# Optimization experiments

Measured on AMD Instinct MI355X. Metric: run time of the kernel, lower is better.

## Reference

```python
import jax, jax.numpy as jnp
import numpy as np

S, B, H, T = 512, 64, 512, 32

def setup_inputs() -> dict:
    key = jax.random.key(0)
    ks = jax.random.split(key, 6)
    hidden = jax.random.normal(ks[0], (S, B, H), jnp.float32)
    lens = jax.random.randint(ks[1], (B,), 1, S + 1)  # sentence lengths in [1, S]
    masks = jnp.ones((S, B), jnp.bool_)  # unused (attention is None), kept for signature parity
    W1 = jax.random.normal(ks[2], (H, H), jnp.float32) / np.sqrt(H)
    b1 = jnp.zeros((H,), jnp.float32)
    W2 = jax.random.normal(ks[3], (H, T), jnp.float32) / np.sqrt(H)
    b2 = jnp.zeros((T,), jnp.float32)
    # xavier_normal_ init for transition
    transition = jax.random.normal(ks[4], (T, T), jnp.float32) * np.sqrt(2.0 / (T + T))
    return {"hidden": hidden, "lens": lens, "masks": masks,
            "W1": W1, "b1": b1, "W2": W2, "b2": b2, "transition": transition}


def _viterbi(emissions, lens, transition):
    # emissions: [S, B, T]; transition[curr, prev]
    Sdim, Bdim, Tn = emissions.shape
    ident = jnp.broadcast_to(jnp.arange(Tn), (Bdim, Tn))  # identity backpointers for padded steps

    def step(fv, inp):
        em_t, t = inp
        scores = fv[:, None, :] + transition[None, :, :]  # [B, curr, prev]
        bp = jnp.argmax(scores, axis=-1)                  # [B, T]
        new_fv = jnp.max(scores, axis=-1) + em_t          # [B, T]
        active = (t < lens)[:, None]
        fv = jnp.where(active, new_fv, fv)                # freeze state past sentence end
        bp = jnp.where(active, bp, ident)
        return fv, bp

    fv0 = emissions[0]
    ts = jnp.arange(1, Sdim)
    fv, bps = jax.lax.scan(step, fv0, (emissions[1:], ts))  # bps: [S-1, B, T]
    best_id = jnp.argmax(fv, axis=-1)   # [B]
    best_score = jnp.max(fv, axis=-1)   # [B]

    def back(tag, bp_t):
        prev = jnp.take_along_axis(bp_t, tag[:, None], axis=1)[:, 0]
        return prev, prev

    _, prevs = jax.lax.scan(back, best_id, bps, reverse=True)  # [S-1, B]
    paths = jnp.concatenate([prevs, best_id[None]], axis=0)    # [S, B]; beyond len-1 the tag repeats
    return paths, best_score


def reference(hidden, lens, masks, W1, b1, W2, b2, transition):
    # hidden2emission: Linear -> Sigmoid -> Linear
    h1 = jax.nn.sigmoid(hidden @ W1 + b1)   # [S, B, H]
    emissions = h1 @ W2 + b2                # [S, B, T]
    paths, best_score = _viterbi(emissions, lens, transition)
    return paths, best_score
```

## Files before the change

### kernel.cpp

```cpp
#include <hip/hip_runtime.h>
#include <math.h>

#define SDIM 512
#define BDIM 64
#define HDIM 512
#define TDIM 32
#define MTOT (SDIM * BDIM)

typedef __attribute__((ext_vector_type(8))) short bf16x8;
typedef __attribute__((ext_vector_type(4))) float f32x4;

__device__ unsigned short g_w1hT[HDIM * HDIM];
__device__ unsigned short g_w1lT[HDIM * HDIM];
__device__ unsigned short g_w2hT[TDIM * HDIM];
__device__ unsigned short g_w2lT[TDIM * HDIM];
__device__ float g_em[(size_t)MTOT * TDIM];

__device__ __forceinline__ unsigned short f2bf(float x) {
  union { float f; unsigned int u; } v; v.f = x;
  unsigned int r = v.u + 0x7FFFu + ((v.u >> 16) & 1u);
  return (unsigned short)(r >> 16);
}
__device__ __forceinline__ float bf2f(unsigned short h) {
  union { float f; unsigned int u; } v; v.u = ((unsigned int)h) << 16; return v.f;
}
__device__ __forceinline__ float fmax3(float a, float b, float c) {
  return fmaxf(fmaxf(a, b), c);
}
__device__ __forceinline__ int imin3(int a, int b, int c) {
  int m = a < b ? a : b; return m < c ? m : c;
}

__global__ void split_kernel(const float* __restrict__ W1, const float* __restrict__ W2) {
  const int n = blockIdx.x;
  const int k0 = threadIdx.x * 4;
  if (n < HDIM) {
    ushort4 h, l; float x;
    x = W1[(size_t)(k0 + 0) * HDIM + n]; h.x = f2bf(x); l.x = f2bf(x - bf2f(h.x));
    x = W1[(size_t)(k0 + 1) * HDIM + n]; h.y = f2bf(x); l.y = f2bf(x - bf2f(h.y));
    x = W1[(size_t)(k0 + 2) * HDIM + n]; h.z = f2bf(x); l.z = f2bf(x - bf2f(h.z));
    x = W1[(size_t)(k0 + 3) * HDIM + n]; h.w = f2bf(x); l.w = f2bf(x - bf2f(h.w));
    *(ushort4*)&g_w1hT[(size_t)n * HDIM + k0] = h;
    *(ushort4*)&g_w1lT[(size_t)n * HDIM + k0] = l;
  } else {
    const int t = n - HDIM;
    ushort4 h, l; float x;
    x = W2[(size_t)(k0 + 0) * TDIM + t]; h.x = f2bf(x); l.x = f2bf(x - bf2f(h.x));
    x = W2[(size_t)(k0 + 1) * TDIM + t]; h.y = f2bf(x); l.y = f2bf(x - bf2f(h.y));
    x = W2[(size_t)(k0 + 2) * TDIM + t]; h.z = f2bf(x); l.z = f2bf(x - bf2f(h.z));
    x = W2[(size_t)(k0 + 3) * TDIM + t]; h.w = f2bf(x); l.w = f2bf(x - bf2f(h.w));
    *(ushort4*)&g_w2hT[(size_t)t * HDIM + k0] = h;
    *(ushort4*)&g_w2lT[(size_t)t * HDIM + k0] = l;
  }
}

__global__ __launch_bounds__(256) void emis_kernel(
    const float* __restrict__ hidden, const float* __restrict__ b1,
    const float* __restrict__ b2)
{
  __shared__ unsigned short lAh[64][40];
  __shared__ unsigned short lAl[64][40];
  __shared__ unsigned short lBh[128][40];
  __shared__ unsigned short lBl[128][40];
  __shared__ unsigned short H1h[64][136];
  __shared__ unsigned short H1l[64][136];

  const int tid = threadIdx.x;
  const int s = blockIdx.x;
  const int row0 = s * 64;
  const int wave = tid >> 6;
  const int lane = tid & 63;
  const int l15 = lane & 15;
  const int l4 = lane >> 4;
  const int wr1 = (wave >> 1) * 32;
  const int wc1 = (wave & 1) * 64;

  f32x4 acc_em[2];
  acc_em[0] = (f32x4)(0.f);
  acc_em[1] = (f32x4)(0.f);

  for (int jcb = 0; jcb < 4; ++jcb) {
    const int jc = jcb * 128;

    f32x4 acc1[2][4];
#pragma unroll
    for (int i = 0; i < 2; ++i)
#pragma unroll
      for (int j = 0; j < 4; ++j) acc1[i][j] = (f32x4)(0.f);

    for (int k0 = 0; k0 < HDIM; k0 += 32) {
#pragma unroll
      for (int i = 0; i < 2; ++i) {
        int f4 = tid + 256 * i;
        int r = f4 >> 3, q = f4 & 7;
        float4 v = *(const float4*)&hidden[(size_t)(row0 + r) * HDIM + k0 + 4 * q];
        ushort4 h, l;
        h.x = f2bf(v.x); l.x = f2bf(v.x - bf2f(h.x));
        h.y = f2bf(v.y); l.y = f2bf(v.y - bf2f(h.y));
        h.z = f2bf(v.z); l.z = f2bf(v.z - bf2f(h.z));
        h.w = f2bf(v.w); l.w = f2bf(v.w - bf2f(h.w));
        *(ushort4*)&lAh[r][4 * q] = h;
        *(ushort4*)&lAl[r][4 * q] = l;
      }
#pragma unroll
      for (int i = 0; i < 2; ++i) {
        int f8 = tid + 256 * i;
        int nl = f8 >> 2, kq8 = f8 & 3;
        *(uint4*)&lBh[nl][8 * kq8] =
            *(const uint4*)&g_w1hT[(size_t)(jc + nl) * HDIM + k0 + 8 * kq8];
        *(uint4*)&lBl[nl][8 * kq8] =
            *(const uint4*)&g_w1lT[(size_t)(jc + nl) * HDIM + k0 + 8 * kq8];
      }
      __syncthreads();

      bf16x8 aH[2], aL[2];
#pragma unroll
      for (int i = 0; i < 2; ++i) {
        aH[i] = *(const bf16x8*)&lAh[wr1 + 16 * i + l15][8 * l4];
        aL[i] = *(const bf16x8*)&lAl[wr1 + 16 * i + l15][8 * l4];
      }
#pragma unroll
      for (int j = 0; j < 4; ++j) {
        bf16x8 bH = *(const bf16x8*)&lBh[wc1 + 16 * j + l15][8 * l4];
        bf16x8 bL = *(const bf16x8*)&lBl[wc1 + 16 * j + l15][8 * l4];
#pragma unroll
        for (int i = 0; i < 2; ++i) {
          acc1[i][j] = __builtin_amdgcn_mfma_f32_16x16x32_bf16(aH[i], bH, acc1[i][j], 0, 0, 0);
          acc1[i][j] = __builtin_amdgcn_mfma_f32_16x16x32_bf16(aH[i], bL, acc1[i][j], 0, 0, 0);
          acc1[i][j] = __builtin_amdgcn_mfma_f32_16x16x32_bf16(aL[i], bH, acc1[i][j], 0, 0, 0);
        }
      }
      __syncthreads();
    }

#pragma unroll
    for (int j = 0; j < 4; ++j) {
      const int col = wc1 + 16 * j + l15;
      const float bv = b1[jc + col];
#pragma unroll
      for (int i = 0; i < 2; ++i) {
#pragma unroll
        for (int r = 0; r < 4; ++r) {
          int lrow = wr1 + 16 * i + 4 * l4 + r;
          float h = 1.f / (1.f + expf(-(acc1[i][j][r] + bv)));
          unsigned short hh = f2bf(h);
          unsigned short hl = f2bf(h - bf2f(hh));
          H1h[lrow][col] = hh;
          H1l[lrow][col] = hl;
        }
      }
    }
    __syncthreads();

#pragma unroll
    for (int ks = 0; ks < 4; ++ks) {
      bf16x8 aH2 = *(const bf16x8*)&H1h[16 * wave + l15][32 * ks + 8 * l4];
      bf16x8 aL2 = *(const bf16x8*)&H1l[16 * wave + l15][32 * ks + 8 * l4];
#pragma unroll
      for (int j2 = 0; j2 < 2; ++j2) {
        const size_t wo = (size_t)(16 * j2 + l15) * HDIM + jc + 32 * ks + 8 * l4;
        bf16x8 bH2 = *(const bf16x8*)&g_w2hT[wo];
        bf16x8 bL2 = *(const bf16x8*)&g_w2lT[wo];
        acc_em[j2] = __builtin_amdgcn_mfma_f32_16x16x32_bf16(aH2, bH2, acc_em[j2], 0, 0, 0);
        acc_em[j2] = __builtin_amdgcn_mfma_f32_16x16x32_bf16(aH2, bL2, acc_em[j2], 0, 0, 0);
        acc_em[j2] = __builtin_amdgcn_mfma_f32_16x16x32_bf16(aL2, bH2, acc_em[j2], 0, 0, 0);
      }
    }
    __syncthreads();
  }

#pragma unroll
  for (int j2 = 0; j2 < 2; ++j2) {
    const int t = 16 * j2 + l15;
    const float bv = b2[t];
#pragma unroll
    for (int r = 0; r < 4; ++r) {
      int b = 16 * wave + 4 * l4 + r;
      g_em[((size_t)b * SDIM + s) * TDIM + t] = acc_em[j2][r] + bv;
    }
  }
}

__global__ __launch_bounds__(64) void viterbi_kernel(
    const int* __restrict__ lens, const float* __restrict__ trans,
    float* __restrict__ out)
{
  __shared__ float fvL[64];
  __shared__ unsigned int bps32[SDIM / 4][TDIM];
  const int b = blockIdx.x;
  const int lane = threadIdx.x;
  const int c = lane & 31;
  const int h = lane >> 5;
  const int p0 = 16 * h;

  float tr[16];
#pragma unroll
  for (int j = 0; j < 16; j += 4) {
    float4 t4 = *(const float4*)&trans[c * TDIM + p0 + j];
    tr[j] = t4.x; tr[j + 1] = t4.y; tr[j + 2] = t4.z; tr[j + 3] = t4.w;
  }

  int len;
  { const int* p32 = lens;
    len = (p32[1] == 0) ? (int)((const long long*)lens)[b] : p32[b]; }

  const float* emc = g_em + (size_t)b * SDIM * TDIM + c;

  float fvown = emc[0];
  fvL[lane] = fvown;

  float ebuf[12];
#pragma unroll
  for (int j = 0; j < 12; ++j) ebuf[j] = emc[(size_t)(1 + j) * TDIM];

  unsigned int bpk = 0u;

#define VSTEP(T, PH, EV)                                                       \
  {                                                                            \
    float4 q0 = *(const float4*)&fvL[p0];                                      \
    float4 q1 = *(const float4*)&fvL[p0 + 4];                                  \
    float4 q2 = *(const float4*)&fvL[p0 + 8];                                  \
    float4 q3 = *(const float4*)&fvL[p0 + 12];                                 \
    float sv[16];                                                              \
    sv[0] = q0.x + tr[0];  sv[1] = q0.y + tr[1];                               \
    sv[2] = q0.z + tr[2];  sv[3] = q0.w + tr[3];                               \
    sv[4] = q1.x + tr[4];  sv[5] = q1.y + tr[5];                               \
    sv[6] = q1.z + tr[6];  sv[7] = q1.w + tr[7];                               \
    sv[8] = q2.x + tr[8];  sv[9] = q2.y + tr[9];                               \
    sv[10] = q2.z + tr[10]; sv[11] = q2.w + tr[11];                            \
    sv[12] = q3.x + tr[12]; sv[13] = q3.y + tr[13];                            \
    sv[14] = q3.z + tr[14]; sv[15] = q3.w + tr[15];                            \
    float l0 = fmax3(sv[0], sv[1], sv[2]);                                     \
    float l1 = fmax3(sv[3], sv[4], sv[5]);                                     \
    float l2 = fmax3(sv[6], sv[7], sv[8]);                                     \
    float l3 = fmax3(sv[9], sv[10], sv[11]);                                   \
    float l4 = fmax3(sv[12], sv[13], sv[14]);                                  \
    float mh = fmaxf(fmax3(l0, l1, l2), fmax3(l3, l4, sv[15]));                \
    float mo = __shfl_xor(mh, 32, 64);                                         \
    float m0 = fmaxf(mh, mo);                                                  \
    const bool act = (T) < len;                                                \
    fvown = act ? (m0 + (EV)) : fvown;                                         \
    fvL[lane] = fvown;       \
    int i_[16];                                                                \
    _Pragma("unroll")                                                          \
    for (int j = 0; j < 16; ++j) i_[j] = (sv[j] == m0) ? j : 63;               \
    int u0 = imin3(i_[0], i_[1], i_[2]);                                       \
    int u1 = imin3(i_[3], i_[4], i_[5]);                                       \
    int u2 = imin3(i_[6], i_[7], i_[8]);                                       \
    int u3 = imin3(i_[9], i_[10], i_[11]);                                     \
    int u4 = imin3(i_[12], i_[13], i_[14]);                                    \
    int jm = imin3(imin3(u0, u1, u2), imin3(u3, u4, i_[15]), 63);              \
    int gi = (jm == 63) ? 255 : (p0 + jm);                                     \
    int go = __shfl_xor(gi, 32, 64);                                           \
    int im = gi < go ? gi : go;                                                \
    int bp = act ? im : c;                                                     \
    bpk |= (unsigned)bp << (8 * (PH));                                         \
    if ((PH) == 3) { bps32[(T) >> 2][c] = bpk; bpk = 0u; }                     \
  }

#define LOADQ(BASE, T0)                                                        \
  {                                                                            \
    _Pragma("unroll")                                                          \
    for (int j = 0; j < 4; ++j) {                                              \
      int lt = (T0) + j; lt = lt > (SDIM - 1) ? (SDIM - 1) : lt;               \
      ebuf[(BASE) + j] = emc[(size_t)lt * TDIM];                               \
    }                                                                          \
  }

  {
    int tq = 1;
    for (; tq <= SDIM - 19; tq += 12) {
      VSTEP(tq + 0, 1, ebuf[0]) VSTEP(tq + 1, 2, ebuf[1])
      VSTEP(tq + 2, 3, ebuf[2]) VSTEP(tq + 3, 0, ebuf[3])
      LOADQ(0, tq + 12)
      VSTEP(tq + 4, 1, ebuf[4]) VSTEP(tq + 5, 2, ebuf[5])
      VSTEP(tq + 6, 3, ebuf[6]) VSTEP(tq + 7, 0, ebuf[7])
      LOADQ(4, tq + 16)
      VSTEP(tq + 8, 1, ebuf[8]) VSTEP(tq + 9, 2, ebuf[9])
      VSTEP(tq + 10, 3, ebuf[10]) VSTEP(tq + 11, 0, ebuf[11])
      LOADQ(8, tq + 20)
    }
    VSTEP(505, 1, ebuf[0]) VSTEP(506, 2, ebuf[1]) VSTEP(507, 3, ebuf[2])
    VSTEP(508, 0, ebuf[3]) VSTEP(509, 1, ebuf[4]) VSTEP(510, 2, ebuf[5])
    VSTEP(511, 3, ebuf[6])
  }
#undef VSTEP
#undef LOADQ

  float bs = fvown;
  int bi = c;
#pragma unroll
  for (int off = 16; off > 0; off >>= 1) {
    float os = __shfl_down(bs, off, 32);
    int oi = __shfl_down(bi, off, 32);
    if (os > bs || (os == bs && oi < bi)) { bs = os; bi = oi; }
  }
  bs = __shfl(bs, 0, 32);
  int tag = __shfl(bi, 0, 32);

  out[(size_t)SDIM * BDIM + b] = bs;
  out[(size_t)(SDIM - 1) * BDIM + b] = (float)tag;

  unsigned bw_next = bps32[SDIM / 4 - 1][c];
  for (int w = SDIM / 4 - 1; w >= 0; --w) {
    unsigned bw = bw_next;
    if (w > 0) bw_next = bps32[w - 1][c];
#pragma unroll
    for (int j = 3; j >= 0; --j) {
      int t = 4 * w + j;
      if (t < 1) continue;
      unsigned word = (unsigned)__builtin_amdgcn_readlane((int)bw, tag);
      tag = (int)((word >> (8 * j)) & 255u);
      out[(size_t)(t - 1) * BDIM + b] = (float)tag;
    }
  }
}

static int find_by_size(const int* in_sizes, int n_in, int sz, int fb) {
  for (int i = 0; i < n_in; ++i) if (in_sizes[i] == sz) return i;
  return fb;
}

extern "C" void kernel_launch(void* const* d_in, const int* in_sizes, int n_in,
                              void* d_out, int out_size, void* d_ws, size_t ws_size,
                              hipStream_t stream) {
  const int i_hidden = find_by_size(in_sizes, n_in, SDIM * BDIM * HDIM, 0);
  const int i_lens   = find_by_size(in_sizes, n_in, BDIM, 1);
  const int i_W1     = find_by_size(in_sizes, n_in, HDIM * HDIM, 3);
  const int i_b1     = find_by_size(in_sizes, n_in, HDIM, 4);
  const int i_W2     = find_by_size(in_sizes, n_in, HDIM * TDIM, 5);
  const int i_b2     = find_by_size(in_sizes, n_in, TDIM, 6);
  const int i_tr     = find_by_size(in_sizes, n_in, TDIM * TDIM, 7);

  const float* hidden = (const float*)d_in[i_hidden];
  const int*   lens   = (const int*)d_in[i_lens];
  const float* W1     = (const float*)d_in[i_W1];
  const float* b1     = (const float*)d_in[i_b1];
  const float* W2     = (const float*)d_in[i_W2];
  const float* b2     = (const float*)d_in[i_b2];
  const float* trans  = (const float*)d_in[i_tr];
  float* out = (float*)d_out;

  split_kernel<<<HDIM + TDIM, 128, 0, stream>>>(W1, W2);
  emis_kernel<<<SDIM, 256, 0, stream>>>(hidden, b1, b2);
  viterbi_kernel<<<BDIM, 64, 0, stream>>>(lens, trans, out);
}
```

Baseline: 239.4 us.

## Pre-split hidden into bf16 hi/lo buffers; widen Viterbi lanes to full row

Adds a split_hidden kernel that converts the whole hidden tensor into bf16 hi/lo arrays once, so the GEMM kernel no longer reconverts the same A tile for each of its four column blocks. The cost is an extra full pass that writes and rereads 64 MB. The sigmoid now uses the fast __expf intrinsic. The Viterbi step has each lane handle all 32 previous tags instead of splitting them across two half-waves, which removes the cross-lane shuffles but doubles per-lane work and leaves half the lanes computing redundantly.

```diff
diff --git a/kernel.cpp b/kernel.cpp
--- a/kernel.cpp
+++ b/kernel.cpp
@@ -14,6 +14,8 @@
 __device__ unsigned short g_w1lT[HDIM * HDIM];
 __device__ unsigned short g_w2hT[TDIM * HDIM];
 __device__ unsigned short g_w2lT[TDIM * HDIM];
+__device__ unsigned short g_aH[(size_t)MTOT * HDIM];
+__device__ unsigned short g_aL[(size_t)MTOT * HDIM];
 __device__ float g_em[(size_t)MTOT * TDIM];
 
 __device__ __forceinline__ unsigned short f2bf(float x) {
@@ -54,9 +56,24 @@
   }
 }
 
+__global__ __launch_bounds__(256) void split_hidden(const float* __restrict__ hidden) {
+  const size_t base = (size_t)blockIdx.x * 4096 + threadIdx.x * 4;
+#pragma unroll
+  for (int i = 0; i < 4; ++i) {
+    size_t idx = base + (size_t)i * 1024;
+    float4 v = *(const float4*)&hidden[idx];
+    ushort4 h, l;
+    h.x = f2bf(v.x); l.x = f2bf(v.x - bf2f(h.x));
+    h.y = f2bf(v.y); l.y = f2bf(v.y - bf2f(h.y));
+    h.z = f2bf(v.z); l.z = f2bf(v.z - bf2f(h.z));
+    h.w = f2bf(v.w); l.w = f2bf(v.w - bf2f(h.w));
+    *(ushort4*)&g_aH[idx] = h;
+    *(ushort4*)&g_aL[idx] = l;
+  }
+}
+
 __global__ __launch_bounds__(256) void emis_kernel(
-    const float* __restrict__ hidden, const float* __restrict__ b1,
-    const float* __restrict__ b2)
+    const float* __restrict__ b1, const float* __restrict__ b2)
 {
   __shared__ unsigned short lAh[64][40];
   __shared__ unsigned short lAl[64][40];
@@ -79,6 +96,8 @@
   acc_em[0] = (f32x4)(0.f);
   acc_em[1] = (f32x4)(0.f);
 
+  const int ar = tid >> 2, aq = tid & 3;
+
   for (int jcb = 0; jcb < 4; ++jcb) {
     const int jc = jcb * 128;
 
@@ -89,18 +108,10 @@
       for (int j = 0; j < 4; ++j) acc1[i][j] = (f32x4)(0.f);
 
     for (int k0 = 0; k0 < HDIM; k0 += 32) {
-#pragma unroll
-      for (int i = 0; i < 2; ++i) {
-        int f4 = tid + 256 * i;
-        int r = f4 >> 3, q = f4 & 7;
-        float4 v = *(const float4*)&hidden[(size_t)(row0 + r) * HDIM + k0 + 4 * q];
-        ushort4 h, l;
-        h.x = f2bf(v.x); l.x = f2bf(v.x - bf2f(h.x));
-        h.y = f2bf(v.y); l.y = f2bf(v.y - bf2f(h.y));
-        h.z = f2bf(v.z); l.z = f2bf(v.z - bf2f(h.z));
-        h.w = f2bf(v.w); l.w = f2bf(v.w - bf2f(h.w));
-        *(ushort4*)&lAh[r][4 * q] = h;
-        *(ushort4*)&lAl[r][4 * q] = l;
+      {
+        const size_t ao = (size_t)(row0 + ar) * HDIM + k0 + 8 * aq;
+        *(uint4*)&lAh[ar][8 * aq] = *(const uint4*)&g_aH[ao];
+        *(uint4*)&lAl[ar][8 * aq] = *(const uint4*)&g_aL[ao];
       }
 #pragma unroll
       for (int i = 0; i < 2; ++i) {
@@ -142,7 +153,7 @@
 #pragma unroll
         for (int r = 0; r < 4; ++r) {
           int lrow = wr1 + 16 * i + 4 * l4 + r;
-          float h = 1.f / (1.f + expf(-(acc1[i][j][r] + bv)));
+          float h = 1.f / (1.f + __expf(-(acc1[i][j][r] + bv)));
           unsigned short hh = f2bf(h);
           unsigned short hl = f2bf(h - bf2f(hh));
           H1h[lrow][col] = hh;
@@ -190,14 +201,12 @@
   const int b = blockIdx.x;
   const int lane = threadIdx.x;
   const int c = lane & 31;
-  const int h = lane >> 5;
-  const int p0 = 16 * h;
-
-  float tr[16];
-#pragma unroll
-  for (int j = 0; j < 16; j += 4) {
-    float4 t4 = *(const float4*)&trans[c * TDIM + p0 + j];
-    tr[j] = t4.x; tr[j + 1] = t4.y; tr[j + 2] = t4.z; tr[j + 3] = t4.w;
+
+  float tr[TDIM];
+#pragma unroll
+  for (int p = 0; p < TDIM; p += 4) {
+    float4 t4 = *(const float4*)&trans[c * TDIM + p];
+    tr[p] = t4.x; tr[p + 1] = t4.y; tr[p + 2] = t4.z; tr[p + 3] = t4.w;
   }
 
   int len;
@@ -217,11 +226,15 @@
 
 #define VSTEP(T, PH, EV)                                                       \
   {                                                                            \
-    float4 q0 = *(const float4*)&fvL[p0];                                      \
-    float4 q1 = *(const float4*)&fvL[p0 + 4];                                  \
-    float4 q2 = *(const float4*)&fvL[p0 + 8];                                  \
-    float4 q3 = *(const float4*)&fvL[p0 + 12];                                 \
-    float sv[16];                                                              \
+    float4 q0 = *(const float4*)&fvL[0];                                       \
+    float4 q1 = *(const float4*)&fvL[4];                                       \
+    float4 q2 = *(const float4*)&fvL[8];                                       \
+    float4 q3 = *(const float4*)&fvL[12];                                      \
+    float4 q4 = *(const float4*)&fvL[16];                                      \
+    float4 q5 = *(const float4*)&fvL[20];                                      \
+    float4 q6 = *(const float4*)&fvL[24];                                      \
+    float4 q7 = *(const float4*)&fvL[28];                                      \
+    float sv[32];                                                              \
     sv[0] = q0.x + tr[0];  sv[1] = q0.y + tr[1];                               \
     sv[2] = q0.z + tr[2];  sv[3] = q0.w + tr[3];                               \
     sv[4] = q1.x + tr[4];  sv[5] = q1.y + tr[5];                               \
@@ -230,29 +243,52 @@
     sv[10] = q2.z + tr[10]; sv[11] = q2.w + tr[11];                            \
     sv[12] = q3.x + tr[12]; sv[13] = q3.y + tr[13];                            \
     sv[14] = q3.z + tr[14]; sv[15] = q3.w + tr[15];                            \
-    float l0 = fmax3(sv[0], sv[1], sv[2]);                                     \
-    float l1 = fmax3(sv[3], sv[4], sv[5]);                                     \
-    float l2 = fmax3(sv[6], sv[7], sv[8]);                                     \
-    float l3 = fmax3(sv[9], sv[10], sv[11]);                                   \
-    float l4 = fmax3(sv[12], sv[13], sv[14]);                                  \
-    float mh = fmaxf(fmax3(l0, l1, l2), fmax3(l3, l4, sv[15]));                \
-    float mo = __shfl_xor(mh, 32, 64);                                         \
-    float m0 = fmaxf(mh, mo);                                                  \
+    sv[16] = q4.x + tr[16]; sv[17] = q4.y + tr[17];                            \
+    sv[18] = q4.z + tr[18]; sv[19] = q4.w + tr[19];                            \
+    sv[20] = q5.x + tr[20]; sv[21] = q5.y + tr[21];                            \
+    sv[22] = q5.z + tr[22]; sv[23] = q5.w + tr[23];                            \
+    sv[24] = q6.x + tr[24]; sv[25] = q6.y + tr[25];                            \
+    sv[26] = q6.z + tr[26]; sv[27] = q6.w + tr[27];                            \
+    sv[28] = q7.x + tr[28]; sv[29] = q7.y + tr[29];                            \
+    sv[30] = q7.z + tr[30]; sv[31] = q7.w + tr[31];                            \
+    float a0 = fmax3(sv[0], sv[1], sv[2]);                                     \
+    float a1 = fmax3(sv[3], sv[4], sv[5]);                                     \
+    float a2 = fmax3(sv[6], sv[7], sv[8]);                                     \
+    float a3 = fmax3(sv[9], sv[10], sv[11]);                                   \
+    float a4 = fmax3(sv[12], sv[13], sv[14]);                                  \
+    float a5 = fmax3(sv[15], sv[16], sv[17]);                                  \
+    float a6 = fmax3(sv[18], sv[19], sv[20]);                                  \
+    float a7 = fmax3(sv[21], sv[22], sv[23]);                                  \
+    float a8 = fmax3(sv[24], sv[25], sv[26]);                                  \
+    float a9 = fmax3(sv[27], sv[28], sv[29]);                                  \
+    float a10 = fmaxf(sv[30], sv[31]);                                         \
+    float b0 = fmax3(a0, a1, a2);                                              \
+    float b1_ = fmax3(a3, a4, a5);                                             \
+    float b2_ = fmax3(a6, a7, a8);                                             \
+    float b3_ = fmaxf(a9, a10);                                                \
+    float m0 = fmaxf(fmaxf(b0, b1_), fmaxf(b2_, b3_));                         \
     const bool act = (T) < len;                                                \
     fvown = act ? (m0 + (EV)) : fvown;                                         \
-    fvL[lane] = fvown;       \
-    int i_[16];                                                                \
+    fvL[lane] = fvown;   \
+    int i_[32];                                                                \
     _Pragma("unroll")                                                          \
-    for (int j = 0; j < 16; ++j) i_[j] = (sv[j] == m0) ? j : 63;               \
+    for (int j = 0; j < 32; ++j) i_[j] = (sv[j] == m0) ? j : 63;               \
     int u0 = imin3(i_[0], i_[1], i_[2]);                                       \
     int u1 = imin3(i_[3], i_[4], i_[5]);                                       \
     int u2 = imin3(i_[6], i_[7], i_[8]);                                       \
     int u3 = imin3(i_[9], i_[10], i_[11]);                                     \
     int u4 = imin3(i_[12], i_[13], i_[14]);                                    \
-    int jm = imin3(imin3(u0, u1, u2), imin3(u3, u4, i_[15]), 63);              \
-    int gi = (jm == 63) ? 255 : (p0 + jm);                                     \
-    int go = __shfl_xor(gi, 32, 64);                                           \
-    int im = gi < go ? gi : go;                                                \
+    int u5 = imin3(i_[15], i_[16], i_[17]);                                    \
+    int u6 = imin3(i_[18], i_[19], i_[20]);                                    \
+    int u7 = imin3(i_[21], i_[22], i_[23]);                                    \
+    int u8 = imin3(i_[24], i_[25], i_[26]);                                    \
+    int u9 = imin3(i_[27], i_[28], i_[29]);                                    \
+    int ua = i_[30] < i_[31] ? i_[30] : i_[31];                                \
+    int w0 = imin3(u0, u1, u2);                                                \
+    int w1 = imin3(u3, u4, u5);                                                \
+    int w2 = imin3(u6, u7, u8);                                                \
+    int w3 = u9 < ua ? u9 : ua;                                                \
+    int im = imin3(w0, w1, w2) < w3 ? imin3(w0, w1, w2) : w3;                  \
     int bp = act ? im : c;                                                     \
     bpk |= (unsigned)bp << (8 * (PH));                                         \
     if ((PH) == 3) { bps32[(T) >> 2][c] = bpk; bpk = 0u; }                     \
@@ -342,6 +378,7 @@
   float* out = (float*)d_out;
 
   split_kernel<<<HDIM + TDIM, 128, 0, stream>>>(W1, W2);
-  emis_kernel<<<SDIM, 256, 0, stream>>>(hidden, b1, b2);
+  split_hidden<<<(MTOT * HDIM) / 4096, 256, 0, stream>>>(hidden);
+  emis_kernel<<<SDIM, 256, 0, stream>>>(b1, b2);
   viterbi_kernel<<<BDIM, 64, 0, stream>>>(lens, trans, out);
 }
```

New measurement: 305.0 us. 27.4% more time.

## Interleave two batch rows per Viterbi wavefront and use fast exp in sigmoid

Applied to the files above, without the earlier changes.

The Viterbi kernel now processes two sentences per 64-lane block, interleaving their independent max/argmax recurrences so each step's LDS, shuffle and ALU latency can overlap across the two chains. Launch count halves to 32 blocks, and backtrace stores are limited to lane 0. The sigmoid in the emission GEMM switches expf to __expf for cheaper transcendental evaluation. The interleaving lengthens each block's dependent chain work and reduces block-level parallelism. The fast exp slightly changes emission precision, which could alter argmax ties.

```diff
diff --git a/kernel.cpp b/kernel.cpp
--- a/kernel.cpp
+++ b/kernel.cpp
@@ -142,7 +142,7 @@
 #pragma unroll
         for (int r = 0; r < 4; ++r) {
           int lrow = wr1 + 16 * i + 4 * l4 + r;
-          float h = 1.f / (1.f + expf(-(acc1[i][j][r] + bv)));
+          float h = 1.f / (1.f + __expf(-(acc1[i][j][r] + bv)));
           unsigned short hh = f2bf(h);
           unsigned short hl = f2bf(h - bf2f(hh));
           H1h[lrow][col] = hh;
@@ -185,13 +185,15 @@
     const int* __restrict__ lens, const float* __restrict__ trans,
     float* __restrict__ out)
 {
-  __shared__ float fvL[64];
-  __shared__ unsigned int bps32[SDIM / 4][TDIM];
-  const int b = blockIdx.x;
+  __shared__ float fvLA[64];
+  __shared__ float fvLB[64];
+  __shared__ unsigned int bps32[2][SDIM / 4][TDIM];
   const int lane = threadIdx.x;
   const int c = lane & 31;
   const int h = lane >> 5;
   const int p0 = 16 * h;
+  const int bA = 2 * blockIdx.x;
+  const int bB = bA + 1;
 
   float tr[16];
 #pragma unroll
@@ -200,62 +202,111 @@
     tr[j] = t4.x; tr[j + 1] = t4.y; tr[j + 2] = t4.z; tr[j + 3] = t4.w;
   }
 
-  int len;
+  int lenA, lenB;
   { const int* p32 = lens;
-    len = (p32[1] == 0) ? (int)((const long long*)lens)[b] : p32[b]; }
-
-  const float* emc = g_em + (size_t)b * SDIM * TDIM + c;
-
-  float fvown = emc[0];
-  fvL[lane] = fvown;
-
-  float ebuf[12];
-#pragma unroll
-  for (int j = 0; j < 12; ++j) ebuf[j] = emc[(size_t)(1 + j) * TDIM];
-
-  unsigned int bpk = 0u;
-
-#define VSTEP(T, PH, EV)                                                       \
+    if (p32[1] == 0) {
+      lenA = (int)((const long long*)lens)[bA];
+      lenB = (int)((const long long*)lens)[bB];
+    } else { lenA = p32[bA]; lenB = p32[bB]; } }
+
+  const float* emcA = g_em + (size_t)bA * SDIM * TDIM + c;
+  const float* emcB = g_em + (size_t)bB * SDIM * TDIM + c;
+
+  float fvA = emcA[0];
+  float fvB = emcB[0];
+  fvLA[lane] = fvA;
+  fvLB[lane] = fvB;
+
+  float ebA[12], ebB[12];
+#pragma unroll
+  for (int j = 0; j < 12; ++j) {
+    ebA[j] = emcA[(size_t)(1 + j) * TDIM];
+    ebB[j] = emcB[(size_t)(1 + j) * TDIM];
+  }
+
+  unsigned int bpkA = 0u, bpkB = 0u;
+
+#define VSTEP(T, PH, EVA, EVB)                                                 \
   {                                                                            \
-    float4 q0 = *(const float4*)&fvL[p0];                                      \
-    float4 q1 = *(const float4*)&fvL[p0 + 4];                                  \
-    float4 q2 = *(const float4*)&fvL[p0 + 8];                                  \
-    float4 q3 = *(const float4*)&fvL[p0 + 12];                                 \
-    float sv[16];                                                              \
-    sv[0] = q0.x + tr[0];  sv[1] = q0.y + tr[1];                               \
-    sv[2] = q0.z + tr[2];  sv[3] = q0.w + tr[3];                               \
-    sv[4] = q1.x + tr[4];  sv[5] = q1.y + tr[5];                               \
-    sv[6] = q1.z + tr[6];  sv[7] = q1.w + tr[7];                               \
-    sv[8] = q2.x + tr[8];  sv[9] = q2.y + tr[9];                               \
-    sv[10] = q2.z + tr[10]; sv[11] = q2.w + tr[11];                            \
-    sv[12] = q3.x + tr[12]; sv[13] = q3.y + tr[13];                            \
-    sv[14] = q3.z + tr[14]; sv[15] = q3.w + tr[15];                            \
-    float l0 = fmax3(sv[0], sv[1], sv[2]);                                     \
-    float l1 = fmax3(sv[3], sv[4], sv[5]);                                     \
-    float l2 = fmax3(sv[6], sv[7], sv[8]);                                     \
-    float l3 = fmax3(sv[9], sv[10], sv[11]);                                   \
-    float l4 = fmax3(sv[12], sv[13], sv[14]);                                  \
-    float mh = fmaxf(fmax3(l0, l1, l2), fmax3(l3, l4, sv[15]));                \
-    float mo = __shfl_xor(mh, 32, 64);                                         \
-    float m0 = fmaxf(mh, mo);                                                  \
-    const bool act = (T) < len;                                                \
-    fvown = act ? (m0 + (EV)) : fvown;                                         \
-    fvL[lane] = fvown;       \
-    int i_[16];                                                                \
+    float4 aq0 = *(const float4*)&fvLA[p0];                                    \
+    float4 aq1 = *(const float4*)&fvLA[p0 + 4];                                \
+    float4 aq2 = *(const float4*)&fvLA[p0 + 8];                                \
+    float4 aq3 = *(const float4*)&fvLA[p0 + 12];                               \
+    float4 bq0 = *(const float4*)&fvLB[p0];                                    \
+    float4 bq1 = *(const float4*)&fvLB[p0 + 4];                                \
+    float4 bq2 = *(const float4*)&fvLB[p0 + 8];                                \
+    float4 bq3 = *(const float4*)&fvLB[p0 + 12];                               \
+    float svA[16], svB[16];                                                    \
+    svA[0] = aq0.x + tr[0];  svA[1] = aq0.y + tr[1];                           \
+    svA[2] = aq0.z + tr[2];  svA[3] = aq0.w + tr[3];                           \
+    svA[4] = aq1.x + tr[4];  svA[5] = aq1.y + tr[5];                           \
+    svA[6] = aq1.z + tr[6];  svA[7] = aq1.w + tr[7];                           \
+    svA[8] = aq2.x + tr[8];  svA[9] = aq2.y + tr[9];                           \
+    svA[10] = aq2.z + tr[10]; svA[11] = aq2.w + tr[11];                        \
+    svA[12] = aq3.x + tr[12]; svA[13] = aq3.y + tr[13];                        \
+    svA[14] = aq3.z + tr[14]; svA[15] = aq3.w + tr[15];                        \
+    svB[0] = bq0.x + tr[0];  svB[1] = bq0.y + tr[1];                           \
+    svB[2] = bq0.z + tr[2];  svB[3] = bq0.w + tr[3];                           \
+    svB[4] = bq1.x + tr[4];  svB[5] = bq1.y + tr[5];                           \
+    svB[6] = bq1.z + tr[6];  svB[7] = bq1.w + tr[7];                           \
+    svB[8] = bq2.x + tr[8];  svB[9] = bq2.y + tr[9];                           \
+    svB[10] = bq2.z + tr[10]; svB[11] = bq2.w + tr[11];                        \
+    svB[12] = bq3.x + tr[12]; svB[13] = bq3.y + tr[13];                        \
+    svB[14] = bq3.z + tr[14]; svB[15] = bq3.w + tr[15];                        \
+    float lA0 = fmax3(svA[0], svA[1], svA[2]);                                 \
+    float lA1 = fmax3(svA[3], svA[4], svA[5]);                                 \
+    float lA2 = fmax3(svA[6], svA[7], svA[8]);                                 \
+    float lA3 = fmax3(svA[9], svA[10], svA[11]);                               \
+    float lA4 = fmax3(svA[12], svA[13], svA[14]);                              \
+    float mhA = fmaxf(fmax3(lA0, lA1, lA2), fmax3(lA3, lA4, svA[15]));         \
+    float lB0 = fmax3(svB[0], svB[1], svB[2]);                                 \
+    float lB1 = fmax3(svB[3], svB[4], svB[5]);                                 \
+    float lB2 = fmax3(svB[6], svB[7], svB[8]);                                 \
+    float lB3 = fmax3(svB[9], svB[10], svB[11]);                               \
+    float lB4 = fmax3(svB[12], svB[13], svB[14]);                              \
+    float mhB = fmaxf(fmax3(lB0, lB1, lB2), fmax3(lB3, lB4, svB[15]));         \
+    float moA = __shfl_xor(mhA, 32, 64);                                       \
+    float moB = __shfl_xor(mhB, 32, 64);                                       \
+    float m0A = fmaxf(mhA, moA);                                               \
+    float m0B = fmaxf(mhB, moB);                                               \
+    const bool actA = (T) < lenA;                                              \
+    const bool actB = (T) < lenB;                                              \
+    fvA = actA ? (m0A + (EVA)) : fvA;                                          \
+    fvB = actB ? (m0B + (EVB)) : fvB;                                          \
+    fvLA[lane] = fvA;                                                          \
+    fvLB[lane] = fvB;                                                          \
+    int iA_[16], iB_[16];                                                      \
     _Pragma("unroll")                                                          \
-    for (int j = 0; j < 16; ++j) i_[j] = (sv[j] == m0) ? j : 63;               \
-    int u0 = imin3(i_[0], i_[1], i_[2]);                                       \
-    int u1 = imin3(i_[3], i_[4], i_[5]);                                       \
-    int u2 = imin3(i_[6], i_[7], i_[8]);                                       \
-    int u3 = imin3(i_[9], i_[10], i_[11]);                                     \
-    int u4 = imin3(i_[12], i_[13], i_[14]);                                    \
-    int jm = imin3(imin3(u0, u1, u2), imin3(u3, u4, i_[15]), 63);              \
-    int gi = (jm == 63) ? 255 : (p0 + jm);                                     \
-    int go = __shfl_xor(gi, 32, 64);                                           \
-    int im = gi < go ? gi : go;                                                \
-    int bp = act ? im : c;                                                     \
-    bpk |= (unsigned)bp << (8 * (PH));                                         \
-    if ((PH) == 3) { bps32[(T) >> 2][c] = bpk; bpk = 0u; }                     \
+    for (int j = 0; j < 16; ++j) iA_[j] = (svA[j] == m0A) ? j : 63;            \
+    _Pragma("unroll")                                                          \
+    for (int j = 0; j < 16; ++j) iB_[j] = (svB[j] == m0B) ? j : 63;            \
+    int uA0 = imin3(iA_[0], iA_[1], iA_[2]);                                   \
+    int uA1 = imin3(iA_[3], iA_[4], iA_[5]);                                   \
+    int uA2 = imin3(iA_[6], iA_[7], iA_[8]);                                   \
+    int uA3 = imin3(iA_[9], iA_[10], iA_[11]);                                 \
+    int uA4 = imin3(iA_[12], iA_[13], iA_[14]);                                \
+    int jmA = imin3(imin3(uA0, uA1, uA2), imin3(uA3, uA4, iA_[15]), 63);       \
+    int uB0 = imin3(iB_[0], iB_[1], iB_[2]);                                   \
+    int uB1 = imin3(iB_[3], iB_[4], iB_[5]);                                   \
+    int uB2 = imin3(iB_[6], iB_[7], iB_[8]);                                   \
+    int uB3 = imin3(iB_[9], iB_[10], iB_[11]);                                 \
+    int uB4 = imin3(iB_[12], iB_[13], iB_[14]);                                \
+    int jmB = imin3(imin3(uB0, uB1, uB2), imin3(uB3, uB4, iB_[15]), 63);       \
+    int giA = (jmA == 63) ? 255 : (p0 + jmA);                                  \
+    int giB = (jmB == 63) ? 255 : (p0 + jmB);                                  \
+    int goA = __shfl_xor(giA, 32, 64);                                         \
+    int goB = __shfl_xor(giB, 32, 64);                                         \
+    int imA = giA < goA ? giA : goA;                                           \
+    int imB = giB < goB ? giB : goB;                                           \
+    int bpA = actA ? imA : c;                                                  \
+    int bpB = actB ? imB : c;                                                  \
+    bpkA |= (unsigned)bpA << (8 * (PH));                                       \
+    bpkB |= (unsigned)bpB << (8 * (PH));                                       \
+    if ((PH) == 3) {                                                           \
+      bps32[0][(T) >> 2][c] = bpkA;                                            \
+      bps32[1][(T) >> 2][c] = bpkB;                                            \
+      bpkA = 0u; bpkB = 0u;                                                    \
+    }                                                                          \
   }
 
 #define LOADQ(BASE, T0)                                                        \
@@ -263,55 +314,71 @@
     _Pragma("unroll")                                                          \
     for (int j = 0; j < 4; ++j) {                                              \
       int lt = (T0) + j; lt = lt > (SDIM - 1) ? (SDIM - 1) : lt;               \
-      ebuf[(BASE) + j] = emc[(size_t)lt * TDIM];                               \
+      ebA[(BASE) + j] = emcA[(size_t)lt * TDIM];                               \
+      ebB[(BASE) + j] = emcB[(size_t)lt * TDIM];                               \
     }                                                                          \
   }
 
   {
     int tq = 1;
     for (; tq <= SDIM - 19; tq += 12) {
-      VSTEP(tq + 0, 1, ebuf[0]) VSTEP(tq + 1, 2, ebuf[1])
-      VSTEP(tq + 2, 3, ebuf[2]) VSTEP(tq + 3, 0, ebuf[3])
+      VSTEP(tq + 0, 1, ebA[0], ebB[0]) VSTEP(tq + 1, 2, ebA[1], ebB[1])
+      VSTEP(tq + 2, 3, ebA[2], ebB[2]) VSTEP(tq + 3, 0, ebA[3], ebB[3])
       LOADQ(0, tq + 12)
-      VSTEP(tq + 4, 1, ebuf[4]) VSTEP(tq + 5, 2, ebuf[5])
-      VSTEP(tq + 6, 3, ebuf[6]) VSTEP(tq + 7, 0, ebuf[7])
+      VSTEP(tq + 4, 1, ebA[4], ebB[4]) VSTEP(tq + 5, 2, ebA[5], ebB[5])
+      VSTEP(tq + 6, 3, ebA[6], ebB[6]) VSTEP(tq + 7, 0, ebA[7], ebB[7])
       LOADQ(4, tq + 16)
-      VSTEP(tq + 8, 1, ebuf[8]) VSTEP(tq + 9, 2, ebuf[9])
-      VSTEP(tq + 10, 3, ebuf[10]) VSTEP(tq + 11, 0, ebuf[11])
+      VSTEP(tq + 8, 1, ebA[8], ebB[8]) VSTEP(tq + 9, 2, ebA[9], ebB[9])
+      VSTEP(tq + 10, 3, ebA[10], ebB[10]) VSTEP(tq + 11, 0, ebA[11], ebB[11])
       LOADQ(8, tq + 20)
     }
-    VSTEP(505, 1, ebuf[0]) VSTEP(506, 2, ebuf[1]) VSTEP(507, 3, ebuf[2])
-    VSTEP(508, 0, ebuf[3]) VSTEP(509, 1, ebuf[4]) VSTEP(510, 2, ebuf[5])
-    VSTEP(511, 3, ebuf[6])
+    VSTEP(505, 1, ebA[0], ebB[0]) VSTEP(506, 2, ebA[1], ebB[1])
+    VSTEP(507, 3, ebA[2], ebB[2]) VSTEP(508, 0, ebA[3], ebB[3])
+    VSTEP(509, 1, ebA[4], ebB[4]) VSTEP(510, 2, ebA[5], ebB[5])
+    VSTEP(511, 3, ebA[6], ebB[6])
   }
 #undef VSTEP
 #undef LOADQ
 
-  float bs = fvown;
-  int bi = c;
+  float bsA = fvA; int biA = c;
+  float bsB = fvB; int biB = c;
 #pragma unroll
   for (int off = 16; off > 0; off >>= 1) {
-    float os = __shfl_down(bs, off, 32);
-    int oi = __shfl_down(bi, off, 32);
-    if (os > bs || (os == bs && oi < bi)) { bs = os; bi = oi; }
-  }
-  bs = __shfl(bs, 0, 32);
-  int tag = __shfl(bi, 0, 32);
-
-  out[(size_t)SDIM * BDIM + b] = bs;
-  out[(size_t)(SDIM - 1) * BDIM + b] = (float)tag;
-
-  unsigned bw_next = bps32[SDIM / 4 - 1][c];
+    float oa = __shfl_down(bsA, off, 32); int ja = __shfl_down(biA, off, 32);
+    if (oa > bsA || (oa == bsA && ja < biA)) { bsA = oa; biA = ja; }
+    float ob = __shfl_down(bsB, off, 32); int jb = __shfl_down(biB, off, 32);
+    if (ob > bsB || (ob == bsB && jb < biB)) { bsB = ob; biB = jb; }
+  }
+  bsA = __shfl(bsA, 0, 64); int tagA = __shfl(biA, 0, 64);
+  bsB = __shfl(bsB, 0, 64); int tagB = __shfl(biB, 0, 64);
+
+  if (lane == 0) {
+    out[(size_t)SDIM * BDIM + bA] = bsA;
+    out[(size_t)SDIM * BDIM + bB] = bsB;
+    out[(size_t)(SDIM - 1) * BDIM + bA] = (float)tagA;
+    out[(size_t)(SDIM - 1) * BDIM + bB] = (float)tagB;
+  }
+
+  unsigned bwAn = bps32[0][SDIM / 4 - 1][c];
+  unsigned bwBn = bps32[1][SDIM / 4 - 1][c];
   for (int w = SDIM / 4 - 1; w >= 0; --w) {
-    unsigned bw = bw_next;
-    if (w > 0) bw_next = bps32[w - 1][c];
+    unsigned bwA = bwAn, bwB = bwBn;
+    if (w > 0) {
+      bwAn = bps32[0][w - 1][c];
+      bwBn = bps32[1][w - 1][c];
+    }
 #pragma unroll
     for (int j = 3; j >= 0; --j) {
       int t = 4 * w + j;
       if (t < 1) continue;
-      unsigned word = (unsigned)__builtin_amdgcn_readlane((int)bw, tag);
-      tag = (int)((word >> (8 * j)) & 255u);
-      out[(size_t)(t - 1) * BDIM + b] = (float)tag;
+      unsigned wa = (unsigned)__builtin_amdgcn_readlane((int)bwA, tagA);
+      unsigned wb = (unsigned)__builtin_amdgcn_readlane((int)bwB, tagB);
+      tagA = (int)((wa >> (8 * j)) & 255u);
+      tagB = (int)((wb >> (8 * j)) & 255u);
+      if (lane == 0) {
+        out[(size_t)(t - 1) * BDIM + bA] = (float)tagA;
+        out[(size_t)(t - 1) * BDIM + bB] = (float)tagB;
+      }
     }
   }
 }
@@ -343,5 +410,5 @@
 
   split_kernel<<<HDIM + TDIM, 128, 0, stream>>>(W1, W2);
   emis_kernel<<<SDIM, 256, 0, stream>>>(hidden, b1, b2);
-  viterbi_kernel<<<BDIM, 64, 0, stream>>>(lens, trans, out);
-}
+  viterbi_kernel<<<BDIM / 2, 64, 0, stream>>>(lens, trans, out);
+}
```

Result: slower. 330.6 us (+38.1%).
